# Performance work log

Measured on AMD Instinct MI355X. Metric: run time of the kernel, lower is better.

Reference implementation:

```python
import jax, jax.numpy as jnp
import numpy as np

D_MODEL = 768
N_HEADS = 12
D_HEAD = D_MODEL // N_HEADS
D_FF = 3072
B, T = 2, 4096
EPS = 1e-5


def _layer_norm(x, gamma, beta):
    mu = jnp.mean(x, axis=-1, keepdims=True)
    var = jnp.var(x, axis=-1, keepdims=True)
    return (x - mu) * jax.lax.rsqrt(var + EPS) * gamma + beta


def setup_inputs() -> dict:
    key = jax.random.key(0)
    ks = jax.random.split(key, 20)
    s = 0.02
    def lin(k, din, dout):
        return jax.random.normal(k, (din, dout), jnp.float32) * s
    inp = {
        "x": jax.random.normal(ks[0], (B, T, D_MODEL), jnp.float32),
        "wq": lin(ks[1], D_MODEL, D_MODEL), "bq": jnp.zeros((D_MODEL,), jnp.float32),
        "wk": lin(ks[2], D_MODEL, D_MODEL), "bk": jnp.zeros((D_MODEL,), jnp.float32),
        "wv": lin(ks[3], D_MODEL, D_MODEL), "bv": jnp.zeros((D_MODEL,), jnp.float32),
        "wo": lin(ks[4], D_MODEL, D_MODEL), "bo": jnp.zeros((D_MODEL,), jnp.float32),
        "w1": lin(ks[5], D_MODEL, D_FF), "b1": jnp.zeros((D_FF,), jnp.float32),
        "w2": lin(ks[6], D_FF, D_MODEL), "b2": jnp.zeros((D_MODEL,), jnp.float32),
        "g1": jnp.ones((D_MODEL,), jnp.float32), "be1": jnp.zeros((D_MODEL,), jnp.float32),
        "g2": jnp.ones((D_MODEL,), jnp.float32), "be2": jnp.zeros((D_MODEL,), jnp.float32),
    }
    return inp


def reference(x, wq, bq, wk, bk, wv, bv, wo, bo, w1, b1, w2, b2, g1, be1, g2, be2):
    Bx, Tx, D = x.shape
    # --- multi-head causal self-attention (naive, full TxT scores) ---
    def split_heads(t):
        return t.reshape(Bx, Tx, N_HEADS, D_HEAD).transpose(0, 2, 1, 3)  # [B,H,T,dh]
    Q = split_heads(x @ wq + bq)
    K = split_heads(x @ wk + bk)
    V = split_heads(x @ wv + bv)
    scores = jnp.einsum("bhqd,bhkd->bhqk", Q, K) / (D_HEAD ** 0.5)
    causal = jnp.tril(jnp.ones((Tx, Tx), bool))
    scores = jnp.where(causal, scores, -jnp.inf)
    weights = jax.nn.softmax(scores, axis=-1)
    attn = jnp.einsum("bhqk,bhkd->bhqd", weights, V)
    attn = attn.transpose(0, 2, 1, 3).reshape(Bx, Tx, D)
    attn_out = attn @ wo + bo
    # --- residual + LN1 ---
    h = _layer_norm(x + attn_out, g1, be1)
    # --- FFN ---
    ffn = jax.nn.relu(h @ w1 + b1) @ w2 + b2
    # --- residual + LN2 ---
    return _layer_norm(h + ffn, g2, be2)
```

## Files before the change

kernel.cpp:

```cpp
#include <hip/hip_runtime.h>
#include <hip/hip_bf16.h>

typedef __hip_bfloat16 bf16;
typedef __attribute__((ext_vector_type(8))) short short8;
typedef __attribute__((ext_vector_type(4))) short short4b;
typedef __attribute__((ext_vector_type(4))) float floatx4;

#define DM   768
#define NH   12
#define DH   64
#define DFF  3072
#define TS   4096
#define NB   2
#define MTOK (NB * TS)
#define EPS  1e-5f
#define NEG  -30000.0f

__device__ __forceinline__ float b2f(bf16 v)  { return __bfloat162float(v); }
__device__ __forceinline__ bf16  f2b(float v) { return __float2bfloat16(v); }
__device__ __forceinline__ short sbf(float x) { bf16 b = __float2bfloat16(x); return *(short*)&b; }
__device__ __forceinline__ float ldf(const float* p) { return *p; }
__device__ __forceinline__ float ldf(const bf16*  p) { return b2f(*p); }
__device__ __forceinline__ void stf(float* p, float v) { *p = v; }
__device__ __forceinline__ void stf(bf16*  p, float v) { *p = f2b(v); }

__device__ __forceinline__ void gl2lds(const bf16* g, short* l) {
    __builtin_amdgcn_global_load_lds(
        (const __attribute__((address_space(1))) void*)g,
        (__attribute__((address_space(3))) void*)l, 16, 0, 0);
}

template <int RELU>
__global__ __launch_bounds__(256)
void gemm_lds(const bf16* __restrict__ A, int lda, const bf16* __restrict__ Wt,
              const float* __restrict__ bias, bf16* __restrict__ C, int ldc,
              int N, int K)
{
    __shared__ __align__(16) short As[128 * 32];
    __shared__ __align__(16) short Bs[128 * 32];

    const int tid  = threadIdx.x;
    const int wave = tid >> 6, lane = tid & 63;
    const int wx = wave & 1, wy = wave >> 1;
    const int quad = lane >> 4, fn = lane & 15;
    const int bm = blockIdx.y * 128, bn = blockIdx.x * 128;
    const int l4 = lane >> 2, l8 = (lane & 3) * 8;

    const bf16* gA0 = A  + (size_t)(bm + wave * 16       + l4) * lda + l8;
    const bf16* gA1 = A  + (size_t)(bm + (wave + 4) * 16 + l4) * lda + l8;
    const bf16* gB0 = Wt + (size_t)(bn + wave * 16       + l4) * K   + l8;
    const bf16* gB1 = Wt + (size_t)(bn + (wave + 4) * 16 + l4) * K   + l8;
    short* lA0 = &As[wave * 512];
    short* lA1 = &As[(wave + 4) * 512];
    short* lB0 = &Bs[wave * 512];
    short* lB1 = &Bs[(wave + 4) * 512];

    floatx4 acc[4][4] = {};

    for (int kk = 0; kk < K; kk += 32) {
        __syncthreads();
        gl2lds(gA0 + kk, lA0);
        gl2lds(gA1 + kk, lA1);
        gl2lds(gB0 + kk, lB0);
        gl2lds(gB1 + kk, lB1);
        __syncthreads();

        short8 af[4], bfr[4];
        #pragma unroll
        for (int i = 0; i < 4; ++i) {
            af[i]  = *(const short8*)&As[(wy * 64 + i * 16 + fn) * 32 + quad * 8];
            bfr[i] = *(const short8*)&Bs[(wx * 64 + i * 16 + fn) * 32 + quad * 8];
        }
        #pragma unroll
        for (int i = 0; i < 4; ++i)
            #pragma unroll
            for (int j = 0; j < 4; ++j)
                acc[i][j] = __builtin_amdgcn_mfma_f32_16x16x32_bf16(
                    af[i], bfr[j], acc[i][j], 0, 0, 0);
    }

    #pragma unroll
    for (int j = 0; j < 4; ++j) {
        const int n = bn + wx * 64 + j * 16 + fn;
        const float bv = bias[n];
        #pragma unroll
        for (int i = 0; i < 4; ++i) {
            #pragma unroll
            for (int rg = 0; rg < 4; ++rg) {
                const int m = bm + wy * 64 + i * 16 + quad * 4 + rg;
                float v = acc[i][j][rg] + bv;
                if (RELU) v = fmaxf(v, 0.f);
                C[(size_t)m * ldc + n] = f2b(v);
            }
        }
    }
}

__global__ __launch_bounds__(256)
void xcvt(const float* __restrict__ x, bf16* __restrict__ xb)
{
    const size_t i = ((size_t)blockIdx.x * 256 + threadIdx.x) * 8;
    const float4 a = *(const float4*)&x[i];
    const float4 b = *(const float4*)&x[i + 4];
    short8 v;
    v[0]=sbf(a.x); v[1]=sbf(a.y); v[2]=sbf(a.z); v[3]=sbf(a.w);
    v[4]=sbf(b.x); v[5]=sbf(b.y); v[6]=sbf(b.z); v[7]=sbf(b.w);
    *(short8*)&xb[i] = v;
}

__global__ __launch_bounds__(256)
void attn_v6(const bf16* __restrict__ QKV, bf16* __restrict__ Out)
{
    __shared__ __align__(16) short Ks[64 * 72];
    __shared__ __align__(16) short Vt[64 * 72];
    __shared__ __align__(16) float Ss[4][16 * 68];
    __shared__ __align__(16) short Ps[4][16 * 72];
    __shared__ float Al[4][16];
    __shared__ float Ll[4][16];

    const int tid  = threadIdx.x;
    const int wave = tid >> 6, lane = tid & 63;
    const int quad = lane >> 4, fn = lane & 15;
    const int bh = blockIdx.y;
    const int b = bh / NH, h = bh % NH;
    const int q0 = (gridDim.x - 1 - blockIdx.x) * 64;
    const int nt = q0 / 64 + 1;
    const int qwmin = q0 + wave * 16;

    const int orow = lane >> 2;
    const int okey = (lane & 3) * 16;

    const short* QKVs = (const short*)QKV;

    const size_t rowQ = (size_t)(b * TS + q0 + wave * 16 + fn) * 2304 + h * 64;
    const short8 qa0 = *(const short8*)&QKV[rowQ + quad * 8];
    const short8 qa1 = *(const short8*)&QKV[rowQ + 32 + quad * 8];

    float mrow = NEG, lrow = 0.f;
    floatx4 o[4] = {};

    const int sk = tid >> 3, sc8 = (tid & 7) * 8;
    const int vd = tid & 63, vk4 = (tid >> 6) * 4;
    const size_t gK = (size_t)(b * TS) * 2304 + 768  + h * 64 + (size_t)sk * 2304 + sc8;
    const size_t gV = (size_t)(b * TS) * 2304 + 1536 + h * 64 + vd;

    short8 kr0 = *(const short8*)&QKVs[gK];
    short8 kr1 = *(const short8*)&QKVs[gK + (size_t)32 * 2304];
    short4b vr0, vr1, vr2, vr3;
    #pragma unroll
    for (int j = 0; j < 4; ++j) {
        vr0[j] = QKVs[gV + (size_t)(vk4 + j) * 2304];
        vr1[j] = QKVs[gV + (size_t)(16 + vk4 + j) * 2304];
        vr2[j] = QKVs[gV + (size_t)(32 + vk4 + j) * 2304];
        vr3[j] = QKVs[gV + (size_t)(48 + vk4 + j) * 2304];
    }

    for (int t = 0; t < nt; ++t) {
        const int kk0 = t * 64;
        __syncthreads();
        *(short8*)&Ks[sk * 72 + sc8]        = kr0;
        *(short8*)&Ks[(sk + 32) * 72 + sc8] = kr1;
        *(short4b*)&Vt[vd * 72 + vk4]       = vr0;
        *(short4b*)&Vt[vd * 72 + 16 + vk4]  = vr1;
        *(short4b*)&Vt[vd * 72 + 32 + vk4]  = vr2;
        *(short4b*)&Vt[vd * 72 + 48 + vk4]  = vr3;
        if (t + 1 < nt) {
            const size_t nk = (size_t)(kk0 + 64) * 2304;
            kr0 = *(const short8*)&QKVs[gK + nk];
            kr1 = *(const short8*)&QKVs[gK + nk + (size_t)32 * 2304];
            #pragma unroll
            for (int j = 0; j < 4; ++j) {
                vr0[j] = QKVs[gV + nk + (size_t)(vk4 + j) * 2304];
                vr1[j] = QKVs[gV + nk + (size_t)(16 + vk4 + j) * 2304];
                vr2[j] = QKVs[gV + nk + (size_t)(32 + vk4 + j) * 2304];
                vr3[j] = QKVs[gV + nk + (size_t)(48 + vk4 + j) * 2304];
            }
        }
        __syncthreads();

        if (kk0 > qwmin + 15) continue;

        __builtin_amdgcn_s_setprio(1);
        floatx4 s[4] = {};
        #pragma unroll
        for (int ks = 0; ks < 4; ++ks) {
            const short8 ka = *(const short8*)&Ks[(ks * 16 + fn) * 72 + quad * 8];
            const short8 kb = *(const short8*)&Ks[(ks * 16 + fn) * 72 + 32 + quad * 8];
            s[ks] = __builtin_amdgcn_mfma_f32_16x16x32_bf16(qa0, ka, s[ks], 0, 0, 0);
            s[ks] = __builtin_amdgcn_mfma_f32_16x16x32_bf16(qa1, kb, s[ks], 0, 0, 0);
        }
        __builtin_amdgcn_s_setprio(0);

        const int qg = q0 + wave * 16 + quad * 4;
        if (kk0 + 63 <= qwmin) {
            #pragma unroll
            for (int ks = 0; ks < 4; ++ks)
                #pragma unroll
                for (int rg = 0; rg < 4; ++rg)
                    Ss[wave][(quad * 4 + rg) * 68 + ks * 16 + fn] = s[ks][rg] * 0.125f;
        } else {
            #pragma unroll
            for (int ks = 0; ks < 4; ++ks)
                #pragma unroll
                for (int rg = 0; rg < 4; ++rg) {
                    const float v = (kk0 + ks * 16 + fn <= qg + rg)
                                        ? s[ks][rg] * 0.125f : NEG;
                    Ss[wave][(quad * 4 + rg) * 68 + ks * 16 + fn] = v;
                }
        }

        float sv[16];
        *(float4*)&sv[0]  = *(const float4*)&Ss[wave][orow * 68 + okey];
        *(float4*)&sv[4]  = *(const float4*)&Ss[wave][orow * 68 + okey + 4];
        *(float4*)&sv[8]  = *(const float4*)&Ss[wave][orow * 68 + okey + 8];
        *(float4*)&sv[12] = *(const float4*)&Ss[wave][orow * 68 + okey + 12];
        float mx = sv[0];
        #pragma unroll
        for (int j = 1; j < 16; ++j) mx = fmaxf(mx, sv[j]);
        mx = fmaxf(mx, __shfl_xor(mx, 1, 64));
        mx = fmaxf(mx, __shfl_xor(mx, 2, 64));
        const float mn2 = fmaxf(mrow, mx);
        float ps = 0.f;
        short8 pb0, pb1;
        #pragma unroll
        for (int j = 0; j < 8; ++j) {
            const float p = __expf(fminf(sv[j] - mn2, 0.f));
            ps += p;
            pb0[j] = sbf(p);
        }
        #pragma unroll
        for (int j = 0; j < 8; ++j) {
            const float p = __expf(fminf(sv[8 + j] - mn2, 0.f));
            ps += p;
            pb1[j] = sbf(p);
        }
        ps += __shfl_xor(ps, 1, 64);
        ps += __shfl_xor(ps, 2, 64);
        const float cr = __expf(fminf(mrow - mn2, 0.f));
        lrow = lrow * cr + ps;
        mrow = mn2;
        *(short8*)&Ps[wave][orow * 72 + okey]     = pb0;
        *(short8*)&Ps[wave][orow * 72 + okey + 8] = pb1;
        if ((lane & 3) == 0) { Al[wave][orow] = cr; Ll[wave][orow] = lrow; }

        float al[4];
        #pragma unroll
        for (int rg = 0; rg < 4; ++rg) al[rg] = Al[wave][quad * 4 + rg];
        #pragma unroll
        for (int cb = 0; cb < 4; ++cb)
            #pragma unroll
            for (int rg = 0; rg < 4; ++rg) o[cb][rg] *= al[rg];
        const short8 pf0 = *(const short8*)&Ps[wave][fn * 72 + quad * 8];
        const short8 pf1 = *(const short8*)&Ps[wave][fn * 72 + 32 + quad * 8];
        __builtin_amdgcn_s_setprio(1);
        #pragma unroll
        for (int cb = 0; cb < 4; ++cb) {
            const short8 vfa = *(const short8*)&Vt[(cb * 16 + fn) * 72 + quad * 8];
            o[cb] = __builtin_amdgcn_mfma_f32_16x16x32_bf16(pf0, vfa, o[cb], 0, 0, 0);
        }
        #pragma unroll
        for (int cb = 0; cb < 4; ++cb) {
            const short8 vfb = *(const short8*)&Vt[(cb * 16 + fn) * 72 + 32 + quad * 8];
            o[cb] = __builtin_amdgcn_mfma_f32_16x16x32_bf16(pf1, vfb, o[cb], 0, 0, 0);
        }
        __builtin_amdgcn_s_setprio(0);
    }

    float li[4];
    #pragma unroll
    for (int rg = 0; rg < 4; ++rg)
        li[rg] = 1.f / fmaxf(Ll[wave][quad * 4 + rg], 1e-20f);
    #pragma unroll
    for (int cb = 0; cb < 4; ++cb)
        #pragma unroll
        for (int rg = 0; rg < 4; ++rg) {
            const size_t row = (size_t)(b * TS + q0 + wave * 16 + quad * 4 + rg);
            Out[row * DM + h * 64 + cb * 16 + fn] = f2b(o[cb][rg] * li[rg]);
        }
}

__global__ __launch_bounds__(256)
void transW(const float* __restrict__ W, bf16* __restrict__ Wt, int K, int N)
{
    __shared__ float t[32][33];
    const int k0 = blockIdx.x * 32, n0 = blockIdx.y * 32;
    const int tx = threadIdx.x, ty = threadIdx.y;
    #pragma unroll
    for (int i = 0; i < 4; ++i)
        t[ty + i * 8][tx] = W[(size_t)(k0 + ty + i * 8) * N + n0 + tx];
    __syncthreads();
    #pragma unroll
    for (int i = 0; i < 4; ++i)
        Wt[(size_t)(n0 + ty + i * 8) * K + k0 + tx] = f2b(t[tx][ty + i * 8]);
}

__global__ __launch_bounds__(256)
void pack_bias(const float* __restrict__ bq, const float* __restrict__ bk,
               const float* __restrict__ bv, float* __restrict__ out)
{
    const int i = blockIdx.x * 256 + threadIdx.x;
    if (i < 3 * DM)
        out[i] = (i < DM) ? bq[i] : (i < 2 * DM) ? bk[i - DM] : bv[i - 2 * DM];
}

template <typename T1, typename T2, typename TOUT>
__global__ __launch_bounds__(256)
void add_ln(const T1* __restrict__ a, const T2* __restrict__ r, int ldr,
            const float* __restrict__ gamma, const float* __restrict__ beta,
            TOUT* __restrict__ out)
{
    const int row = blockIdx.x;
    const size_t offa = (size_t)row * DM;
    const size_t offr = (size_t)row * ldr;
    const int tid = threadIdx.x;

    float v[3];
    float s = 0.f, s2 = 0.f;
    #pragma unroll
    for (int j = 0; j < 3; ++j) {
        const int i = tid + j * 256;
        const float t = ldf(a + offa + i) + ldf(r + offr + i);
        v[j] = t; s += t; s2 += t * t;
    }
    __shared__ float red[256], red2[256];
    red[tid] = s; red2[tid] = s2;
    __syncthreads();
    #pragma unroll
    for (int st = 128; st > 0; st >>= 1) {
        if (tid < st) { red[tid] += red[tid + st]; red2[tid] += red2[tid + st]; }
        __syncthreads();
    }
    const float mu   = red[0] * (1.f / DM);
    const float var  = red2[0] * (1.f / DM) - mu * mu;
    const float rstd = rsqrtf(var + EPS);
    #pragma unroll
    for (int j = 0; j < 3; ++j) {
        const int i = tid + j * 256;
        stf(out + offa + i, (v[j] - mu) * rstd * gamma[i] + beta[i]);
    }
}

extern "C" void kernel_launch(void* const* d_in, const int* in_sizes, int n_in,
                              void* d_out, int out_size, void* d_ws, size_t ws_size,
                              hipStream_t stream)
{
    (void)in_sizes; (void)n_in; (void)out_size; (void)ws_size;

    const float* x   = (const float*)d_in[0];
    const float* wq  = (const float*)d_in[1];  const float* bq  = (const float*)d_in[2];
    const float* wk  = (const float*)d_in[3];  const float* bk  = (const float*)d_in[4];
    const float* wv  = (const float*)d_in[5];  const float* bv  = (const float*)d_in[6];
    const float* wo  = (const float*)d_in[7];  const float* bo  = (const float*)d_in[8];
    const float* w1  = (const float*)d_in[9];  const float* b1  = (const float*)d_in[10];
    const float* w2  = (const float*)d_in[11]; const float* b2  = (const float*)d_in[12];
    const float* g1  = (const float*)d_in[13]; const float* be1 = (const float*)d_in[14];
    const float* g2  = (const float*)d_in[15]; const float* be2 = (const float*)d_in[16];

    const size_t S = (size_t)MTOK * DM;
    bf16* QKVb = (bf16*)d_ws;
    bf16* Hb   = QKVb + 3 * S;
    bf16* wbuf = Hb + S;
    float* bqkv = (float*)(wbuf + (size_t)2 * DFF * DM);
    bf16* F1 = QKVb;
    bf16* Yb = QKVb + 2 * S;
    bf16* Pb = QKVb + DM;
    bf16* Ao = Hb;
    bf16* xb = Hb;

    const dim3 tblk(32, 8);
    const dim3 blk(256);

    xcvt<<<dim3(3072), blk, 0, stream>>>(x, xb);

    transW<<<dim3(24, 24), tblk, 0, stream>>>(wq, wbuf,                    DM, DM);
    transW<<<dim3(24, 24), tblk, 0, stream>>>(wk, wbuf + (size_t)DM * DM,  DM, DM);
    transW<<<dim3(24, 24), tblk, 0, stream>>>(wv, wbuf + (size_t)2*DM*DM,  DM, DM);
    pack_bias<<<dim3(9), blk, 0, stream>>>(bq, bk, bv, bqkv);
    gemm_lds<0><<<dim3(18, 64), blk, 0, stream>>>(
        xb, DM, wbuf, bqkv, QKVb, 3 * DM, 3 * DM, DM);

    attn_v6<<<dim3(64, NB * NH), blk, 0, stream>>>(QKVb, Ao);

    transW<<<dim3(24, 24), tblk, 0, stream>>>(wo, wbuf, DM, DM);
    gemm_lds<0><<<dim3(6, 64), blk, 0, stream>>>(
        Ao, DM, wbuf, bo, Pb, 3 * DM, DM, DM);
    add_ln<float, bf16, bf16><<<dim3(MTOK), blk, 0, stream>>>(
        x, Pb, 3 * DM, g1, be1, Hb);

    transW<<<dim3(24, 96), tblk, 0, stream>>>(w1, wbuf, DM, DFF);
    bf16* w2t = wbuf + (size_t)DFF * DM;
    transW<<<dim3(96, 24), tblk, 0, stream>>>(w2, w2t, DFF, DM);
    for (int m0 = 0; m0 < MTOK; m0 += 4096) {
        gemm_lds<1><<<dim3(24, 32), blk, 0, stream>>>(
            Hb + (size_t)m0 * DM, DM, wbuf, b1, F1, DFF, DFF, DM);
        gemm_lds<0><<<dim3(6, 32), blk, 0, stream>>>(
            F1, DFF, w2t, b2, Yb + (size_t)m0 * DM, DM, DM, DFF);
    }

    add_ln<bf16, bf16, float><<<dim3(MTOK), blk, 0, stream>>>(
        Hb, Yb, DM, g2, be2, (float*)d_out);
}
```

Before: 685.5 us.

## Process two 64-row query tiles per attention block to reuse K/V loads

The attention kernel now handles 128 query rows per block as two 64-row sub-tiles (A and B), with one shared K/V tile load in LDS feeding both. This halves the grid and roughly halves K/V global traffic and LDS staging per query row. The diagonal tiles are handled by compile-time-specialised variants for masking. In exchange, register and LDS use per block rise, fewer blocks run, and causal imbalance across blocks may grow.

```diff
diff --git a/kernel.cpp b/kernel.cpp
--- a/kernel.cpp
+++ b/kernel.cpp
@@ -24,6 +24,9 @@
 __device__ __forceinline__ void stf(float* p, float v) { *p = v; }
 __device__ __forceinline__ void stf(bf16*  p, float v) { *p = f2b(v); }
 
+struct TagT { static constexpr bool v = true;  };
+struct TagF { static constexpr bool v = false; };
+
 __device__ __forceinline__ void gl2lds(const bf16* g, short* l) {
     __builtin_amdgcn_global_load_lds(
         (const __attribute__((address_space(1))) void*)g,
@@ -109,35 +112,37 @@
 }
 
 __global__ __launch_bounds__(256)
-void attn_v6(const bf16* __restrict__ QKV, bf16* __restrict__ Out)
+void attn_v7(const bf16* __restrict__ QKV, bf16* __restrict__ Out)
 {
     __shared__ __align__(16) short Ks[64 * 72];
     __shared__ __align__(16) short Vt[64 * 72];
-    __shared__ __align__(16) float Ss[4][16 * 68];
-    __shared__ __align__(16) short Ps[4][16 * 72];
-    __shared__ float Al[4][16];
-    __shared__ float Ll[4][16];
+    __shared__ __align__(16) float Ss[2][4][16 * 68];
+    __shared__ __align__(16) short Ps[2][4][16 * 72];
+    __shared__ float Al[2][4][16];
+    __shared__ float Ll[2][4][16];
 
     const int tid  = threadIdx.x;
     const int wave = tid >> 6, lane = tid & 63;
     const int quad = lane >> 4, fn = lane & 15;
     const int bh = blockIdx.y;
     const int b = bh / NH, h = bh % NH;
-    const int q0 = (gridDim.x - 1 - blockIdx.x) * 64;
-    const int nt = q0 / 64 + 1;
-    const int qwmin = q0 + wave * 16;
+    const int q0 = (gridDim.x - 1 - blockIdx.x) * 128;
+    const int nt = q0 / 64 + 2;
 
     const int orow = lane >> 2;
     const int okey = (lane & 3) * 16;
 
     const short* QKVs = (const short*)QKV;
 
-    const size_t rowQ = (size_t)(b * TS + q0 + wave * 16 + fn) * 2304 + h * 64;
-    const short8 qa0 = *(const short8*)&QKV[rowQ + quad * 8];
-    const short8 qa1 = *(const short8*)&QKV[rowQ + 32 + quad * 8];
-
-    float mrow = NEG, lrow = 0.f;
-    floatx4 o[4] = {};
+    const size_t rowQA = (size_t)(b * TS + q0 + wave * 16 + fn) * 2304 + h * 64;
+    const size_t rowQB = rowQA + (size_t)64 * 2304;
+    const short8 qaA0 = *(const short8*)&QKV[rowQA + quad * 8];
+    const short8 qaA1 = *(const short8*)&QKV[rowQA + 32 + quad * 8];
+    const short8 qaB0 = *(const short8*)&QKV[rowQB + quad * 8];
+    const short8 qaB1 = *(const short8*)&QKV[rowQB + 32 + quad * 8];
+
+    float mrA = NEG, lrA = 0.f, mrB = NEG, lrB = 0.f;
+    floatx4 oA[4] = {}, oB[4] = {};
 
     const int sk = tid >> 3, sc8 = (tid & 7) * 8;
     const int vd = tid & 63, vk4 = (tid >> 6) * 4;
@@ -178,104 +183,195 @@
         }
         __syncthreads();
 
-        if (kk0 > qwmin + 15) continue;
-
-        __builtin_amdgcn_s_setprio(1);
-        floatx4 s[4] = {};
+        short8 ka[4], kb[4];
         #pragma unroll
         for (int ks = 0; ks < 4; ++ks) {
-            const short8 ka = *(const short8*)&Ks[(ks * 16 + fn) * 72 + quad * 8];
-            const short8 kb = *(const short8*)&Ks[(ks * 16 + fn) * 72 + 32 + quad * 8];
-            s[ks] = __builtin_amdgcn_mfma_f32_16x16x32_bf16(qa0, ka, s[ks], 0, 0, 0);
-            s[ks] = __builtin_amdgcn_mfma_f32_16x16x32_bf16(qa1, kb, s[ks], 0, 0, 0);
+            ka[ks] = *(const short8*)&Ks[(ks * 16 + fn) * 72 + quad * 8];
+            kb[ks] = *(const short8*)&Ks[(ks * 16 + fn) * 72 + 32 + quad * 8];
         }
-        __builtin_amdgcn_s_setprio(0);
-
-        const int qg = q0 + wave * 16 + quad * 4;
-        if (kk0 + 63 <= qwmin) {
-            #pragma unroll
-            for (int ks = 0; ks < 4; ++ks)
-                #pragma unroll
-                for (int rg = 0; rg < 4; ++rg)
-                    Ss[wave][(quad * 4 + rg) * 68 + ks * 16 + fn] = s[ks][rg] * 0.125f;
-        } else {
-            #pragma unroll
-            for (int ks = 0; ks < 4; ++ks)
-                #pragma unroll
-                for (int rg = 0; rg < 4; ++rg) {
-                    const float v = (kk0 + ks * 16 + fn <= qg + rg)
-                                        ? s[ks][rg] * 0.125f : NEG;
-                    Ss[wave][(quad * 4 + rg) * 68 + ks * 16 + fn] = v;
-                }
-        }
-
-        float sv[16];
-        *(float4*)&sv[0]  = *(const float4*)&Ss[wave][orow * 68 + okey];
-        *(float4*)&sv[4]  = *(const float4*)&Ss[wave][orow * 68 + okey + 4];
-        *(float4*)&sv[8]  = *(const float4*)&Ss[wave][orow * 68 + okey + 8];
-        *(float4*)&sv[12] = *(const float4*)&Ss[wave][orow * 68 + okey + 12];
-        float mx = sv[0];
-        #pragma unroll
-        for (int j = 1; j < 16; ++j) mx = fmaxf(mx, sv[j]);
-        mx = fmaxf(mx, __shfl_xor(mx, 1, 64));
-        mx = fmaxf(mx, __shfl_xor(mx, 2, 64));
-        const float mn2 = fmaxf(mrow, mx);
-        float ps = 0.f;
-        short8 pb0, pb1;
-        #pragma unroll
-        for (int j = 0; j < 8; ++j) {
-            const float p = __expf(fminf(sv[j] - mn2, 0.f));
-            ps += p;
-            pb0[j] = sbf(p);
-        }
-        #pragma unroll
-        for (int j = 0; j < 8; ++j) {
-            const float p = __expf(fminf(sv[8 + j] - mn2, 0.f));
-            ps += p;
-            pb1[j] = sbf(p);
-        }
-        ps += __shfl_xor(ps, 1, 64);
-        ps += __shfl_xor(ps, 2, 64);
-        const float cr = __expf(fminf(mrow - mn2, 0.f));
-        lrow = lrow * cr + ps;
-        mrow = mn2;
-        *(short8*)&Ps[wave][orow * 72 + okey]     = pb0;
-        *(short8*)&Ps[wave][orow * 72 + okey + 8] = pb1;
-        if ((lane & 3) == 0) { Al[wave][orow] = cr; Ll[wave][orow] = lrow; }
-
-        float al[4];
-        #pragma unroll
-        for (int rg = 0; rg < 4; ++rg) al[rg] = Al[wave][quad * 4 + rg];
-        #pragma unroll
-        for (int cb = 0; cb < 4; ++cb)
-            #pragma unroll
-            for (int rg = 0; rg < 4; ++rg) o[cb][rg] *= al[rg];
-        const short8 pf0 = *(const short8*)&Ps[wave][fn * 72 + quad * 8];
-        const short8 pf1 = *(const short8*)&Ps[wave][fn * 72 + 32 + quad * 8];
-        __builtin_amdgcn_s_setprio(1);
-        #pragma unroll
-        for (int cb = 0; cb < 4; ++cb) {
-            const short8 vfa = *(const short8*)&Vt[(cb * 16 + fn) * 72 + quad * 8];
-            o[cb] = __builtin_amdgcn_mfma_f32_16x16x32_bf16(pf0, vfa, o[cb], 0, 0, 0);
-        }
-        #pragma unroll
-        for (int cb = 0; cb < 4; ++cb) {
-            const short8 vfb = *(const short8*)&Vt[(cb * 16 + fn) * 72 + 32 + quad * 8];
-            o[cb] = __builtin_amdgcn_mfma_f32_16x16x32_bf16(pf1, vfb, o[cb], 0, 0, 0);
-        }
-        __builtin_amdgcn_s_setprio(0);
-    }
-
-    float li[4];
-    #pragma unroll
-    for (int rg = 0; rg < 4; ++rg)
-        li[rg] = 1.f / fmaxf(Ll[wave][quad * 4 + rg], 1e-20f);
+
+        auto tile = [&](auto actT, auto adiagT) {
+            constexpr bool ACT   = decltype(actT)::v;
+            constexpr bool ADIAG = decltype(adiagT)::v;
+
+            __builtin_amdgcn_s_setprio(1);
+            floatx4 sB[4] = {};
+            #pragma unroll
+            for (int ks = 0; ks < 4; ++ks) {
+                sB[ks] = __builtin_amdgcn_mfma_f32_16x16x32_bf16(qaB0, ka[ks], sB[ks], 0, 0, 0);
+                sB[ks] = __builtin_amdgcn_mfma_f32_16x16x32_bf16(qaB1, kb[ks], sB[ks], 0, 0, 0);
+            }
+            floatx4 sA[4] = {};
+            if constexpr (ACT) {
+                #pragma unroll
+                for (int ks = 0; ks < 4; ++ks) {
+                    sA[ks] = __builtin_amdgcn_mfma_f32_16x16x32_bf16(qaA0, ka[ks], sA[ks], 0, 0, 0);
+                    sA[ks] = __builtin_amdgcn_mfma_f32_16x16x32_bf16(qaA1, kb[ks], sA[ks], 0, 0, 0);
+                }
+            }
+            __builtin_amdgcn_s_setprio(0);
+
+            if constexpr (ACT) {
+                #pragma unroll
+                for (int ks = 0; ks < 4; ++ks)
+                    #pragma unroll
+                    for (int rg = 0; rg < 4; ++rg)
+                        Ss[1][wave][(quad * 4 + rg) * 68 + ks * 16 + fn] = sB[ks][rg] * 0.125f;
+            } else {
+                const int qgB = q0 + 64 + wave * 16 + quad * 4;
+                #pragma unroll
+                for (int ks = 0; ks < 4; ++ks)
+                    #pragma unroll
+                    for (int rg = 0; rg < 4; ++rg) {
+                        const float v = (kk0 + ks * 16 + fn <= qgB + rg)
+                                            ? sB[ks][rg] * 0.125f : NEG;
+                        Ss[1][wave][(quad * 4 + rg) * 68 + ks * 16 + fn] = v;
+                    }
+            }
+            if constexpr (ACT) {
+                if constexpr (ADIAG) {
+                    const int qgA = q0 + wave * 16 + quad * 4;
+                    #pragma unroll
+                    for (int ks = 0; ks < 4; ++ks)
+                        #pragma unroll
+                        for (int rg = 0; rg < 4; ++rg) {
+                            const float v = (kk0 + ks * 16 + fn <= qgA + rg)
+                                                ? sA[ks][rg] * 0.125f : NEG;
+                            Ss[0][wave][(quad * 4 + rg) * 68 + ks * 16 + fn] = v;
+                        }
+                } else {
+                    #pragma unroll
+                    for (int ks = 0; ks < 4; ++ks)
+                        #pragma unroll
+                        for (int rg = 0; rg < 4; ++rg)
+                            Ss[0][wave][(quad * 4 + rg) * 68 + ks * 16 + fn] = sA[ks][rg] * 0.125f;
+                }
+            }
+
+            float svB[16];
+            *(float4*)&svB[0]  = *(const float4*)&Ss[1][wave][orow * 68 + okey];
+            *(float4*)&svB[4]  = *(const float4*)&Ss[1][wave][orow * 68 + okey + 4];
+            *(float4*)&svB[8]  = *(const float4*)&Ss[1][wave][orow * 68 + okey + 8];
+            *(float4*)&svB[12] = *(const float4*)&Ss[1][wave][orow * 68 + okey + 12];
+            float svA[16];
+            if constexpr (ACT) {
+                *(float4*)&svA[0]  = *(const float4*)&Ss[0][wave][orow * 68 + okey];
+                *(float4*)&svA[4]  = *(const float4*)&Ss[0][wave][orow * 68 + okey + 4];
+                *(float4*)&svA[8]  = *(const float4*)&Ss[0][wave][orow * 68 + okey + 8];
+                *(float4*)&svA[12] = *(const float4*)&Ss[0][wave][orow * 68 + okey + 12];
+            }
+
+            {
+                float mx = svB[0];
+                #pragma unroll
+                for (int j = 1; j < 16; ++j) mx = fmaxf(mx, svB[j]);
+                mx = fmaxf(mx, __shfl_xor(mx, 1, 64));
+                mx = fmaxf(mx, __shfl_xor(mx, 2, 64));
+                const float mn2 = fmaxf(mrB, mx);
+                float ps = 0.f;
+                short8 pb0, pb1;
+                #pragma unroll
+                for (int j = 0; j < 8; ++j) {
+                    const float p = __expf(fminf(svB[j] - mn2, 0.f));
+                    ps += p; pb0[j] = sbf(p);
+                }
+                #pragma unroll
+                for (int j = 0; j < 8; ++j) {
+                    const float p = __expf(fminf(svB[8 + j] - mn2, 0.f));
+                    ps += p; pb1[j] = sbf(p);
+                }
+                ps += __shfl_xor(ps, 1, 64);
+                ps += __shfl_xor(ps, 2, 64);
+                const float cr = __expf(fminf(mrB - mn2, 0.f));
+                lrB = lrB * cr + ps;
+                mrB = mn2;
+                *(short8*)&Ps[1][wave][orow * 72 + okey]     = pb0;
+                *(short8*)&Ps[1][wave][orow * 72 + okey + 8] = pb1;
+                if ((lane & 3) == 0) { Al[1][wave][orow] = cr; Ll[1][wave][orow] = lrB; }
+            }
+            if constexpr (ACT) {
+                float mx = svA[0];
+                #pragma unroll
+                for (int j = 1; j < 16; ++j) mx = fmaxf(mx, svA[j]);
+                mx = fmaxf(mx, __shfl_xor(mx, 1, 64));
+                mx = fmaxf(mx, __shfl_xor(mx, 2, 64));
+                const float mn2 = fmaxf(mrA, mx);
+                float ps = 0.f;
+                short8 pb0, pb1;
+                #pragma unroll
+                for (int j = 0; j < 8; ++j) {
+                    const float p = __expf(fminf(svA[j] - mn2, 0.f));
+                    ps += p; pb0[j] = sbf(p);
+                }
+                #pragma unroll
+                for (int j = 0; j < 8; ++j) {
+                    const float p = __expf(fminf(svA[8 + j] - mn2, 0.f));
+                    ps += p; pb1[j] = sbf(p);
+                }
+                ps += __shfl_xor(ps, 1, 64);
+                ps += __shfl_xor(ps, 2, 64);
+                const float cr = __expf(fminf(mrA - mn2, 0.f));
+                lrA = lrA * cr + ps;
+                mrA = mn2;
+                *(short8*)&Ps[0][wave][orow * 72 + okey]     = pb0;
+                *(short8*)&Ps[0][wave][orow * 72 + okey + 8] = pb1;
+                if ((lane & 3) == 0) { Al[0][wave][orow] = cr; Ll[0][wave][orow] = lrA; }
+            }
+
+            float alB[4];
+            #pragma unroll
+            for (int rg = 0; rg < 4; ++rg) alB[rg] = Al[1][wave][quad * 4 + rg];
+            #pragma unroll
+            for (int cb = 0; cb < 4; ++cb)
+                #pragma unroll
+                for (int rg = 0; rg < 4; ++rg) oB[cb][rg] *= alB[rg];
+            const short8 pfB0 = *(const short8*)&Ps[1][wave][fn * 72 + quad * 8];
+            const short8 pfB1 = *(const short8*)&Ps[1][wave][fn * 72 + 32 + quad * 8];
+            short8 pfA0, pfA1;
+            if constexpr (ACT) {
+                float alA[4];
+                #pragma unroll
+                for (int rg = 0; rg < 4; ++rg) alA[rg] = Al[0][wave][quad * 4 + rg];
+                #pragma unroll
+                for (int cb = 0; cb < 4; ++cb)
+                    #pragma unroll
+                    for (int rg = 0; rg < 4; ++rg) oA[cb][rg] *= alA[rg];
+                pfA0 = *(const short8*)&Ps[0][wave][fn * 72 + quad * 8];
+                pfA1 = *(const short8*)&Ps[0][wave][fn * 72 + 32 + quad * 8];
+            }
+            __builtin_amdgcn_s_setprio(1);
+            #pragma unroll
+            for (int cb = 0; cb < 4; ++cb) {
+                const short8 vfa = *(const short8*)&Vt[(cb * 16 + fn) * 72 + quad * 8];
+                const short8 vfb = *(const short8*)&Vt[(cb * 16 + fn) * 72 + 32 + quad * 8];
+                oB[cb] = __builtin_amdgcn_mfma_f32_16x16x32_bf16(pfB0, vfa, oB[cb], 0, 0, 0);
+                oB[cb] = __builtin_amdgcn_mfma_f32_16x16x32_bf16(pfB1, vfb, oB[cb], 0, 0, 0);
+                if constexpr (ACT) {
+                    oA[cb] = __builtin_amdgcn_mfma_f32_16x16x32_bf16(pfA0, vfa, oA[cb], 0, 0, 0);
+                    oA[cb] = __builtin_amdgcn_mfma_f32_16x16x32_bf16(pfA1, vfb, oA[cb], 0, 0, 0);
+                }
+            }
+            __builtin_amdgcn_s_setprio(0);
+        };
+
+        if (t < nt - 2)       tile(TagT{}, TagF{});
+        else if (t == nt - 2) tile(TagT{}, TagT{});
+        else                  tile(TagF{}, TagF{});
+    }
+
+    float liA[4], liB[4];
+    #pragma unroll
+    for (int rg = 0; rg < 4; ++rg) {
+        liA[rg] = 1.f / fmaxf(Ll[0][wave][quad * 4 + rg], 1e-20f);
+        liB[rg] = 1.f / fmaxf(Ll[1][wave][quad * 4 + rg], 1e-20f);
+    }
     #pragma unroll
     for (int cb = 0; cb < 4; ++cb)
         #pragma unroll
         for (int rg = 0; rg < 4; ++rg) {
-            const size_t row = (size_t)(b * TS + q0 + wave * 16 + quad * 4 + rg);
-            Out[row * DM + h * 64 + cb * 16 + fn] = f2b(o[cb][rg] * li[rg]);
+            const size_t rowA = (size_t)(b * TS + q0 + wave * 16 + quad * 4 + rg);
+            Out[rowA * DM + h * 64 + cb * 16 + fn] = f2b(oA[cb][rg] * liA[rg]);
+            Out[(rowA + 64) * DM + h * 64 + cb * 16 + fn] = f2b(oB[cb][rg] * liB[rg]);
         }
 }
 
@@ -379,7 +475,7 @@
     gemm_lds<0><<<dim3(18, 64), blk, 0, stream>>>(
         xb, DM, wbuf, bqkv, QKVb, 3 * DM, 3 * DM, DM);
 
-    attn_v6<<<dim3(64, NB * NH), blk, 0, stream>>>(QKVb, Ao);
+    attn_v7<<<dim3(32, NB * NH), blk, 0, stream>>>(QKVb, Ao);
 
     transW<<<dim3(24, 24), tblk, 0, stream>>>(wo, wbuf, DM, DM);
     gemm_lds<0><<<dim3(6, 64), blk, 0, stream>>>(
```

New measurement: 786.1 us. 1.15x slower.
